# Optimization experiments

Measured on AMD Instinct MI355X. Metric: run time of the kernel, lower is better.

## Reference

```python
import jax, jax.numpy as jnp
import numpy as np

NUM_EMBEDDINGS = 512
EMBEDDING_DIM = 64
COMMITMENT_COST = 0.25


def setup_inputs() -> dict:
    key = jax.random.key(0)
    k1, k2 = jax.random.split(key)
    x = jax.random.normal(k1, (32, EMBEDDING_DIM, 64, 64), dtype=jnp.float32)
    # nn.Embedding weight initialized uniform(-1/K, 1/K)
    codebook = jax.random.uniform(
        k2, (NUM_EMBEDDINGS, EMBEDDING_DIM), dtype=jnp.float32,
        minval=-1.0 / NUM_EMBEDDINGS, maxval=1.0 / NUM_EMBEDDINGS)
    return {"x": x, "codebook": codebook}


def reference(x, codebook):
    # x: [B, C, H, W] with C == embedding_dim; codebook: [K, C]
    inputs = jnp.transpose(x, (0, 2, 3, 1))  # [B, H, W, C]
    in_shape = inputs.shape
    flat = inputs.reshape(-1, codebook.shape[1])  # [N, C]
    # squared L2 distances: ||z||^2 + ||e||^2 - 2 z.e
    distances = (jnp.sum(flat * flat, axis=1, keepdims=True)
                 + jnp.sum(codebook * codebook, axis=1)
                 - 2.0 * jnp.matmul(flat, codebook.T))  # [N, K]
    idx = jnp.argmin(distances, axis=1)  # [N]
    quantized = codebook[idx].reshape(in_shape)  # [B, H, W, C]
    e_latent_loss = jnp.mean((jax.lax.stop_gradient(quantized) - inputs) ** 2)
    q_latent_loss = jnp.mean((quantized - jax.lax.stop_gradient(inputs)) ** 2)
    loss = q_latent_loss + COMMITMENT_COST * e_latent_loss
    # straight-through estimator
    quantized = inputs + jax.lax.stop_gradient(quantized - inputs)
    quantized = jnp.transpose(quantized, (0, 3, 1, 2))  # back to [B, C, H, W]
    return quantized, loss
```

## Files before the change

kernel.cpp:

```cpp
#include <hip/hip_runtime.h>

typedef __bf16 bf16x8 __attribute__((ext_vector_type(8)));
typedef float  f32x16 __attribute__((ext_vector_type(16)));

#define HW      4096
#define CDIM    64
#define KCODES  512
#define PBLK    512
#define TPB     512
#define NPOS    131072


__global__ __launch_bounds__(TPB, 2)
void vqvae_kernel(const float* __restrict__ x,
                  const float* __restrict__ cb,
                  float* __restrict__ out,
                  float* __restrict__ loss_out)
{
    __shared__ bf16x8 cbB[16][4][64];
    __shared__ bf16x8 zB [16][4][64];
    __shared__ float    ecb[KCODES];
    __shared__ unsigned minu[PBLK];
    __shared__ float    red[8];

    const int t   = threadIdx.x;
    const int l   = t & 63;
    const int w   = t >> 6;
    const int n0  = blockIdx.x * PBLK;
    const int b   = n0 >> 12;
    const int hw0 = n0 & (HW - 1);

    #pragma unroll
    for (int j = 0; j < 8; ++j) {
        int slot  = t + TPB * j;
        int lane  = slot & 63;
        int s     = (slot >> 6) & 3;
        int chunk = slot >> 8;
        int code  = chunk * 32 + (lane & 31);
        int c0    = s * 16 + (lane >> 5) * 8;
        const float4* p = (const float4*)(cb + code * CDIM + c0);
        float4 a0 = p[0], a1 = p[1];
        bf16x8 v;
        v[0] = (__bf16)(-2.0f * a0.x); v[1] = (__bf16)(-2.0f * a0.y);
        v[2] = (__bf16)(-2.0f * a0.z); v[3] = (__bf16)(-2.0f * a0.w);
        v[4] = (__bf16)(-2.0f * a1.x); v[5] = (__bf16)(-2.0f * a1.y);
        v[6] = (__bf16)(-2.0f * a1.z); v[7] = (__bf16)(-2.0f * a1.w);
        cbB[chunk][s][lane] = v;
    }

    {
        const float4* p = (const float4*)(cb + t * CDIM);
        float ssum = 0.f;
        #pragma unroll
        for (int q4 = 0; q4 < 16; ++q4) {
            float4 a = p[q4];
            ssum = fmaf(a.x, a.x, ssum); ssum = fmaf(a.y, a.y, ssum);
            ssum = fmaf(a.z, a.z, ssum); ssum = fmaf(a.w, a.w, ssum);
        }
        ecb[t] = 1.0f + ssum;
    }

    float zsq = 0.f;
    {
        const float* xb = x + (b * CDIM) * HW + hw0 + t;
        #pragma unroll
        for (int s = 0; s < 4; ++s)
        #pragma unroll
        for (int h = 0; h < 2; ++h) {
            bf16x8 v;
            #pragma unroll
            for (int i = 0; i < 8; ++i) {
                float f = xb[(s * 16 + h * 8 + i) * HW];
                zsq = fmaf(f, f, zsq);
                v[i] = (__bf16)f;
            }
            zB[t >> 5][s][(t & 31) + 32 * h] = v;
        }
    }
    __syncthreads();

    bf16x8 az[2][4];
    #pragma unroll
    for (int g = 0; g < 2; ++g)
        #pragma unroll
        for (int s = 0; s < 4; ++s)
            az[g][s] = zB[2 * w + g][s][l];

    unsigned urun[2][16];
    #pragma unroll
    for (int g = 0; g < 2; ++g)
        #pragma unroll
        for (int i = 0; i < 16; ++i)
            urun[g][i] = 0xFFFFFFFFu;

    for (int chunk = 0; chunk < 16; ++chunk) {
        bf16x8 bb0 = cbB[chunk][0][l];
        bf16x8 bb1 = cbB[chunk][1][l];
        bf16x8 bb2 = cbB[chunk][2][l];
        bf16x8 bb3 = cbB[chunk][3][l];
        float bias = ecb[chunk * 32 + (l & 31)];
        f32x16 acc0, acc1;
        #pragma unroll
        for (int i = 0; i < 16; ++i) { acc0[i] = bias; acc1[i] = bias; }
        acc0 = __builtin_amdgcn_mfma_f32_32x32x16_bf16(az[0][0], bb0, acc0, 0, 0, 0);
        acc1 = __builtin_amdgcn_mfma_f32_32x32x16_bf16(az[1][0], bb0, acc1, 0, 0, 0);
        acc0 = __builtin_amdgcn_mfma_f32_32x32x16_bf16(az[0][1], bb1, acc0, 0, 0, 0);
        acc1 = __builtin_amdgcn_mfma_f32_32x32x16_bf16(az[1][1], bb1, acc1, 0, 0, 0);
        acc0 = __builtin_amdgcn_mfma_f32_32x32x16_bf16(az[0][2], bb2, acc0, 0, 0, 0);
        acc1 = __builtin_amdgcn_mfma_f32_32x32x16_bf16(az[1][2], bb2, acc1, 0, 0, 0);
        acc0 = __builtin_amdgcn_mfma_f32_32x32x16_bf16(az[0][3], bb3, acc0, 0, 0, 0);
        acc1 = __builtin_amdgcn_mfma_f32_32x32x16_bf16(az[1][3], bb3, acc1, 0, 0, 0);
        unsigned kor = (unsigned)(chunk * 32 + (l & 31));
        #pragma unroll
        for (int i = 0; i < 16; ++i) {
            unsigned u0 = (__float_as_uint(acc0[i]) & 0xFFFFFE00u) | kor;
            unsigned u1 = (__float_as_uint(acc1[i]) & 0xFFFFFE00u) | kor;
            urun[0][i] = (u0 < urun[0][i]) ? u0 : urun[0][i];
            urun[1][i] = (u1 < urun[1][i]) ? u1 : urun[1][i];
        }
    }

    #pragma unroll
    for (int g = 0; g < 2; ++g)
        #pragma unroll
        for (int i = 0; i < 16; ++i) {
            unsigned u = urun[g][i];
            #pragma unroll
            for (int m = 1; m <= 16; m <<= 1) {
                unsigned o = __shfl_xor(u, m, 64);
                u = (o < u) ? o : u;
            }
            urun[g][i] = u;
        }
    if ((l & 31) == 0) {
        int h = l >> 5;
        #pragma unroll
        for (int g = 0; g < 2; ++g)
            #pragma unroll
            for (int i = 0; i < 16; ++i)
                minu[(2 * w + g) * 32 + (i & 3) + 8 * (i >> 2) + 4 * h] = urun[g][i];
    }
    __syncthreads();

    unsigned u = minu[t];
    int   k      = (int)(u & 511u);
    float sprime = __uint_as_float(u & 0xFFFFFE00u);
    float lossv  = zsq + (sprime - 1.0f);

    {
        float* ob = out + (b * CDIM) * HW + hw0 + t;
        int chunk = k >> 5;
        int klane = k & 31;
        #pragma unroll
        for (int s = 0; s < 4; ++s)
        #pragma unroll
        for (int h = 0; h < 2; ++h) {
            bf16x8 q = cbB[chunk][s][klane + 32 * h];
            #pragma unroll
            for (int i = 0; i < 8; ++i)
                ob[(s * 16 + h * 8 + i) * HW] = -0.5f * (float)q[i];
        }
    }

    #pragma unroll
    for (int m = 1; m < 64; m <<= 1)
        lossv += __shfl_xor(lossv, m, 64);
    if (l == 0) red[w] = lossv;
    __syncthreads();
    if (t == 0) {
        float tot = 0.f;
        #pragma unroll
        for (int i = 0; i < 8; ++i) tot += red[i];
        atomicAdd(loss_out, tot * (1.25f / 8388608.0f));
    }
}

extern "C" void kernel_launch(void* const* d_in, const int* in_sizes, int n_in,
                              void* d_out, int out_size, void* d_ws, size_t ws_size,
                              hipStream_t stream) {
    const float* x   = (const float*)d_in[0];
    const float* cb  = (const float*)d_in[1];
    float* out  = (float*)d_out;
    float* loss = out + (out_size - 1);
    hipMemsetAsync(loss, 0, sizeof(float), stream);
    vqvae_kernel<<<dim3(NPOS / PBLK), dim3(TPB), 0, stream>>>(x, cb, out, loss);
}
```

Before: 103.6 us.

## Switch distance MFMA to FP8 with scaled codebook and halve block size

Quantizes the input vectors and the scaled codebook (-512x) to FP8 and uses the 32x32x16 fp8 MFMA in place of bf16, rescaling the bias and loss. The output values are reconstructed from the FP8 codebook copy, and the block is halved to 256 positions and threads. This is meant to cut the LDS footprint and MFMA and conversion cost. It risks wrong argmin choices and a quantized output far less accurate than bf16. The kernel is likely memory-bound, so the compute savings may not matter.

```diff
diff --git a/kernel.cpp b/kernel.cpp
--- a/kernel.cpp
+++ b/kernel.cpp
@@ -1,13 +1,12 @@
 #include <hip/hip_runtime.h>
 
-typedef __bf16 bf16x8 __attribute__((ext_vector_type(8)));
-typedef float  f32x16 __attribute__((ext_vector_type(16)));
+typedef float f32x16 __attribute__((ext_vector_type(16)));
 
 #define HW      4096
 #define CDIM    64
 #define KCODES  512
-#define PBLK    512
-#define TPB     512
+#define PBLK    256
+#define TPB     256
 #define NPOS    131072
 
 
@@ -17,11 +16,11 @@
                   float* __restrict__ out,
                   float* __restrict__ loss_out)
 {
-    __shared__ bf16x8 cbB[16][4][64];
-    __shared__ bf16x8 zB [16][4][64];
+    __shared__ unsigned long long cbB[16][4][64];
+    __shared__ unsigned long long zB [8][4][64];
     __shared__ float    ecb[KCODES];
     __shared__ unsigned minu[PBLK];
-    __shared__ float    red[8];
+    __shared__ float    red[4];
 
     const int t   = threadIdx.x;
     const int l   = t & 63;
@@ -31,7 +30,7 @@
     const int hw0 = n0 & (HW - 1);
 
     #pragma unroll
-    for (int j = 0; j < 8; ++j) {
+    for (int j = 0; j < 16; ++j) {
         int slot  = t + TPB * j;
         int lane  = slot & 63;
         int s     = (slot >> 6) & 3;
@@ -40,16 +39,19 @@
         int c0    = s * 16 + (lane >> 5) * 8;
         const float4* p = (const float4*)(cb + code * CDIM + c0);
         float4 a0 = p[0], a1 = p[1];
-        bf16x8 v;
-        v[0] = (__bf16)(-2.0f * a0.x); v[1] = (__bf16)(-2.0f * a0.y);
-        v[2] = (__bf16)(-2.0f * a0.z); v[3] = (__bf16)(-2.0f * a0.w);
-        v[4] = (__bf16)(-2.0f * a1.x); v[5] = (__bf16)(-2.0f * a1.y);
-        v[6] = (__bf16)(-2.0f * a1.z); v[7] = (__bf16)(-2.0f * a1.w);
-        cbB[chunk][s][lane] = v;
-    }
-
-    {
-        const float4* p = (const float4*)(cb + t * CDIM);
+        int w0, w1;
+        w0 = __builtin_amdgcn_cvt_pk_fp8_f32(-512.f * a0.x, -512.f * a0.y, 0,  false);
+        w0 = __builtin_amdgcn_cvt_pk_fp8_f32(-512.f * a0.z, -512.f * a0.w, w0, true);
+        w1 = __builtin_amdgcn_cvt_pk_fp8_f32(-512.f * a1.x, -512.f * a1.y, 0,  false);
+        w1 = __builtin_amdgcn_cvt_pk_fp8_f32(-512.f * a1.z, -512.f * a1.w, w1, true);
+        cbB[chunk][s][lane] =
+            ((unsigned long long)(unsigned)w1 << 32) | (unsigned long long)(unsigned)w0;
+    }
+
+    #pragma unroll
+    for (int r = 0; r < 2; ++r) {
+        int code = t + r * TPB;
+        const float4* p = (const float4*)(cb + code * CDIM);
         float ssum = 0.f;
         #pragma unroll
         for (int q4 = 0; q4 < 16; ++q4) {
@@ -57,7 +59,7 @@
             ssum = fmaf(a.x, a.x, ssum); ssum = fmaf(a.y, a.y, ssum);
             ssum = fmaf(a.z, a.z, ssum); ssum = fmaf(a.w, a.w, ssum);
         }
-        ecb[t] = 1.0f + ssum;
+        ecb[code] = 128.0f + 256.0f * ssum;
     }
 
     float zsq = 0.f;
@@ -67,85 +69,88 @@
         for (int s = 0; s < 4; ++s)
         #pragma unroll
         for (int h = 0; h < 2; ++h) {
-            bf16x8 v;
+            float f[8];
             #pragma unroll
             for (int i = 0; i < 8; ++i) {
-                float f = xb[(s * 16 + h * 8 + i) * HW];
-                zsq = fmaf(f, f, zsq);
-                v[i] = (__bf16)f;
+                f[i] = xb[(s * 16 + h * 8 + i) * HW];
+                zsq = fmaf(f[i], f[i], zsq);
             }
-            zB[t >> 5][s][(t & 31) + 32 * h] = v;
+            int w0, w1;
+            w0 = __builtin_amdgcn_cvt_pk_fp8_f32(f[0], f[1], 0,  false);
+            w0 = __builtin_amdgcn_cvt_pk_fp8_f32(f[2], f[3], w0, true);
+            w1 = __builtin_amdgcn_cvt_pk_fp8_f32(f[4], f[5], 0,  false);
+            w1 = __builtin_amdgcn_cvt_pk_fp8_f32(f[6], f[7], w1, true);
+            zB[t >> 5][s][(t & 31) + 32 * h] =
+                ((unsigned long long)(unsigned)w1 << 32) | (unsigned long long)(unsigned)w0;
         }
     }
     __syncthreads();
 
-    bf16x8 az[2][4];
-    #pragma unroll
-    for (int g = 0; g < 2; ++g)
-        #pragma unroll
-        for (int s = 0; s < 4; ++s)
-            az[g][s] = zB[2 * w + g][s][l];
-
-    unsigned urun[2][16];
-    #pragma unroll
-    for (int g = 0; g < 2; ++g)
-        #pragma unroll
-        for (int i = 0; i < 16; ++i)
-            urun[g][i] = 0xFFFFFFFFu;
+    long az0[4], az1[4];
+    #pragma unroll
+    for (int s = 0; s < 4; ++s) {
+        az0[s] = (long)zB[2 * w + 0][s][l];
+        az1[s] = (long)zB[2 * w + 1][s][l];
+    }
+
+    unsigned urun0[16], urun1[16];
+    #pragma unroll
+    for (int i = 0; i < 16; ++i) { urun0[i] = 0xFFFFFFFFu; urun1[i] = 0xFFFFFFFFu; }
 
     for (int chunk = 0; chunk < 16; ++chunk) {
-        bf16x8 bb0 = cbB[chunk][0][l];
-        bf16x8 bb1 = cbB[chunk][1][l];
-        bf16x8 bb2 = cbB[chunk][2][l];
-        bf16x8 bb3 = cbB[chunk][3][l];
+        long b0 = (long)cbB[chunk][0][l];
+        long b1 = (long)cbB[chunk][1][l];
+        long b2 = (long)cbB[chunk][2][l];
+        long b3 = (long)cbB[chunk][3][l];
         float bias = ecb[chunk * 32 + (l & 31)];
         f32x16 acc0, acc1;
         #pragma unroll
         for (int i = 0; i < 16; ++i) { acc0[i] = bias; acc1[i] = bias; }
-        acc0 = __builtin_amdgcn_mfma_f32_32x32x16_bf16(az[0][0], bb0, acc0, 0, 0, 0);
-        acc1 = __builtin_amdgcn_mfma_f32_32x32x16_bf16(az[1][0], bb0, acc1, 0, 0, 0);
-        acc0 = __builtin_amdgcn_mfma_f32_32x32x16_bf16(az[0][1], bb1, acc0, 0, 0, 0);
-        acc1 = __builtin_amdgcn_mfma_f32_32x32x16_bf16(az[1][1], bb1, acc1, 0, 0, 0);
-        acc0 = __builtin_amdgcn_mfma_f32_32x32x16_bf16(az[0][2], bb2, acc0, 0, 0, 0);
-        acc1 = __builtin_amdgcn_mfma_f32_32x32x16_bf16(az[1][2], bb2, acc1, 0, 0, 0);
-        acc0 = __builtin_amdgcn_mfma_f32_32x32x16_bf16(az[0][3], bb3, acc0, 0, 0, 0);
-        acc1 = __builtin_amdgcn_mfma_f32_32x32x16_bf16(az[1][3], bb3, acc1, 0, 0, 0);
+        acc0 = __builtin_amdgcn_mfma_f32_32x32x16_fp8_fp8(az0[0], b0, acc0, 0, 0, 0);
+        acc1 = __builtin_amdgcn_mfma_f32_32x32x16_fp8_fp8(az1[0], b0, acc1, 0, 0, 0);
+        acc0 = __builtin_amdgcn_mfma_f32_32x32x16_fp8_fp8(az0[1], b1, acc0, 0, 0, 0);
+        acc1 = __builtin_amdgcn_mfma_f32_32x32x16_fp8_fp8(az1[1], b1, acc1, 0, 0, 0);
+        acc0 = __builtin_amdgcn_mfma_f32_32x32x16_fp8_fp8(az0[2], b2, acc0, 0, 0, 0);
+        acc1 = __builtin_amdgcn_mfma_f32_32x32x16_fp8_fp8(az1[2], b2, acc1, 0, 0, 0);
+        acc0 = __builtin_amdgcn_mfma_f32_32x32x16_fp8_fp8(az0[3], b3, acc0, 0, 0, 0);
+        acc1 = __builtin_amdgcn_mfma_f32_32x32x16_fp8_fp8(az1[3], b3, acc1, 0, 0, 0);
         unsigned kor = (unsigned)(chunk * 32 + (l & 31));
         #pragma unroll
         for (int i = 0; i < 16; ++i) {
             unsigned u0 = (__float_as_uint(acc0[i]) & 0xFFFFFE00u) | kor;
             unsigned u1 = (__float_as_uint(acc1[i]) & 0xFFFFFE00u) | kor;
-            urun[0][i] = (u0 < urun[0][i]) ? u0 : urun[0][i];
-            urun[1][i] = (u1 < urun[1][i]) ? u1 : urun[1][i];
-        }
-    }
-
-    #pragma unroll
-    for (int g = 0; g < 2; ++g)
-        #pragma unroll
-        for (int i = 0; i < 16; ++i) {
-            unsigned u = urun[g][i];
-            #pragma unroll
-            for (int m = 1; m <= 16; m <<= 1) {
-                unsigned o = __shfl_xor(u, m, 64);
-                u = (o < u) ? o : u;
-            }
-            urun[g][i] = u;
-        }
+            urun0[i] = (u0 < urun0[i]) ? u0 : urun0[i];
+            urun1[i] = (u1 < urun1[i]) ? u1 : urun1[i];
+        }
+    }
+
+    #pragma unroll
+    for (int i = 0; i < 16; ++i) {
+        unsigned u0 = urun0[i], u1 = urun1[i];
+        #pragma unroll
+        for (int m = 1; m <= 16; m <<= 1) {
+            unsigned o0 = __shfl_xor(u0, m, 64);
+            unsigned o1 = __shfl_xor(u1, m, 64);
+            u0 = (o0 < u0) ? o0 : u0;
+            u1 = (o1 < u1) ? o1 : u1;
+        }
+        urun0[i] = u0; urun1[i] = u1;
+    }
     if ((l & 31) == 0) {
         int h = l >> 5;
         #pragma unroll
-        for (int g = 0; g < 2; ++g)
-            #pragma unroll
-            for (int i = 0; i < 16; ++i)
-                minu[(2 * w + g) * 32 + (i & 3) + 8 * (i >> 2) + 4 * h] = urun[g][i];
+        for (int i = 0; i < 16; ++i) {
+            int r = (i & 3) + 8 * (i >> 2) + 4 * h;
+            minu[(2 * w + 0) * 32 + r] = urun0[i];
+            minu[(2 * w + 1) * 32 + r] = urun1[i];
+        }
     }
     __syncthreads();
 
     unsigned u = minu[t];
     int   k      = (int)(u & 511u);
     float sprime = __uint_as_float(u & 0xFFFFFE00u);
-    float lossv  = zsq + (sprime - 1.0f);
+    float lossv  = zsq + (sprime - 128.0f) * (1.0f / 256.0f);
 
     {
         float* ob = out + (b * CDIM) * HW + hw0 + t;
@@ -155,10 +160,21 @@
         for (int s = 0; s < 4; ++s)
         #pragma unroll
         for (int h = 0; h < 2; ++h) {
-            bf16x8 q = cbB[chunk][s][klane + 32 * h];
+            unsigned long long q = cbB[chunk][s][klane + 32 * h];
+            int qlo = (int)(unsigned)(q & 0xFFFFFFFFull);
+            int qhi = (int)(unsigned)(q >> 32);
+            float v[8];
+            v[0] = __builtin_amdgcn_cvt_f32_fp8(qlo, 0);
+            v[1] = __builtin_amdgcn_cvt_f32_fp8(qlo, 1);
+            v[2] = __builtin_amdgcn_cvt_f32_fp8(qlo, 2);
+            v[3] = __builtin_amdgcn_cvt_f32_fp8(qlo, 3);
+            v[4] = __builtin_amdgcn_cvt_f32_fp8(qhi, 0);
+            v[5] = __builtin_amdgcn_cvt_f32_fp8(qhi, 1);
+            v[6] = __builtin_amdgcn_cvt_f32_fp8(qhi, 2);
+            v[7] = __builtin_amdgcn_cvt_f32_fp8(qhi, 3);
             #pragma unroll
             for (int i = 0; i < 8; ++i)
-                ob[(s * 16 + h * 8 + i) * HW] = -0.5f * (float)q[i];
+                ob[(s * 16 + h * 8 + i) * HW] = v[i] * (-1.0f / 512.0f);
         }
     }
 
@@ -168,9 +184,7 @@
     if (l == 0) red[w] = lossv;
     __syncthreads();
     if (t == 0) {
-        float tot = 0.f;
-        #pragma unroll
-        for (int i = 0; i < 8; ++i) tot += red[i];
+        float tot = red[0] + red[1] + red[2] + red[3];
         atomicAdd(loss_out, tot * (1.25f / 8388608.0f));
     }
 }
```

Measured after the change: 107.8 us. 4.1% more time.
